# Performance work log

Measured on AMD Instinct MI355X. Metric: run time of the kernel, lower is better.

## Reference

```python
import jax, jax.numpy as jnp
import numpy as np

B = 4096
D = 512
TEMPERATURE = 0.07


def setup_inputs() -> dict:
    key = jax.random.key(0)
    k1, k2 = jax.random.split(key)
    logits = jax.random.normal(k1, (B, D), dtype=jnp.float32)
    label = jax.random.normal(k2, (B, D), dtype=jnp.float32)
    return {"logits": logits, "label": label}


def reference(logits, label):
    # concat the two views -> [2B, D]
    feats = jnp.concatenate([logits, label], axis=0)
    n = feats.shape[0]
    b = n // 2
    # L2 normalize along feature dim (F.normalize, eps for safety)
    norm = jnp.maximum(jnp.linalg.norm(feats, axis=1, keepdims=True), 1e-12)
    feats = feats / norm
    # similarity matrix [2B, 2B]
    sim = jnp.matmul(feats, feats.T) / TEMPERATURE
    idx = jnp.arange(n)
    # positive pair of row i is row (i + B) mod 2B
    pos = sim[idx, (idx + b) % n]
    # CrossEntropy with target 0 over [pos, negatives] == masked LSE - pos.
    # Mask out the diagonal (self-similarity), which the torch code removes
    # via the boolean-eye mask before building logits.
    neg_inf = jnp.array(-jnp.inf, dtype=sim.dtype)
    sim_masked = jnp.where(idx[:, None] == idx[None, :], neg_inf, sim)
    lse = jax.nn.logsumexp(sim_masked, axis=1)
    loss = jnp.mean(lse - pos)
    return loss
```

## Files before the change

### kernel.cpp

```cpp
#include <hip/hip_runtime.h>
#include <hip/hip_bf16.h>

#define NROWS 8192
#define BHALF 4096
#define DDIM  512

#define BM 256
#define BK 64
#define KT (DDIM / BK)
#define NT (NROWS / BM)
#define NTRI (NT * (NT + 1) / 2)
#define NFULL 512
#define NHALFB 32
#define GRID (NFULL + NHALFB)

#define FSCALE 3.7796447300922722f

typedef short bf16x8 __attribute__((ext_vector_type(8)));
typedef float f32x4 __attribute__((ext_vector_type(4)));
typedef unsigned short u16x8 __attribute__((ext_vector_type(8)));
typedef __attribute__((address_space(1))) unsigned int gu32;
typedef __attribute__((address_space(3))) unsigned int lu32;

#define MFMA_(a, b, c) __builtin_amdgcn_mfma_f32_16x16x32_bf16(a, b, c, 0, 0, 0)
#define VMCNT(N) asm volatile("s_waitcnt vmcnt(" #N ")" ::: "memory")
#define LGKM0                                            \
  do {                                                   \
    asm volatile("s_waitcnt lgkmcnt(0)" ::: "memory");   \
    __builtin_amdgcn_sched_barrier(0);                   \
  } while (0)
#define BAR                                              \
  do {                                                   \
    __builtin_amdgcn_sched_barrier(0);                   \
    __builtin_amdgcn_s_barrier();                        \
    __builtin_amdgcn_sched_barrier(0);                   \
  } while (0)

__global__ __launch_bounds__(256) void normalize_kernel(
    const float* __restrict__ logits, const float* __restrict__ label,
    unsigned short* __restrict__ fn, float* __restrict__ rowsum,
    float* __restrict__ out) {
  if (blockIdx.x < 8)
    ((float4*)rowsum)[blockIdx.x * 256 + threadIdx.x] =
        make_float4(0.f, 0.f, 0.f, 0.f);
  if (blockIdx.x == 8 && threadIdx.x == 0) out[0] = 0.f;

  const int w = threadIdx.x >> 6, lane = threadIdx.x & 63;
  const int row = blockIdx.x * 4 + w;
  const float* src = (row < BHALF) ? (logits + (size_t)row * DDIM)
                                   : (label + (size_t)(row - BHALF) * DDIM);
  const float4* s4 = (const float4*)src;
  float4 a = s4[lane * 2 + 0];
  float4 b = s4[lane * 2 + 1];
  float ss = a.x * a.x + a.y * a.y + a.z * a.z + a.w * a.w +
             b.x * b.x + b.y * b.y + b.z * b.z + b.w * b.w;
#pragma unroll
  for (int m = 1; m < 64; m <<= 1) ss += __shfl_xor(ss, m);
  const float inv = FSCALE / fmaxf(sqrtf(ss), 1e-12f);
  const float v[8] = {a.x, a.y, a.z, a.w, b.x, b.y, b.z, b.w};
  u16x8 o;
#pragma unroll
  for (int j = 0; j < 8; ++j) {
    float x = v[j] * inv;
    unsigned u = __float_as_uint(x);
    unsigned r = (u + 0x7fffu + ((u >> 16) & 1u)) >> 16;
    o[j] = (unsigned short)r;
  }
  *(u16x8*)(fn + (size_t)row * DDIM + lane * 8) = o;
}

template <int BN_>
__device__ __attribute__((always_inline)) void tile_body(
    const unsigned short* __restrict__ fn, float* __restrict__ rowsum,
    float* __restrict__ pos, int rowBase, int colBase) {
  extern __shared__ char lds[];
  __shared__ float lds_rsum[BM];
  __shared__ float lds_csum[BM];
  constexpr int NFRAG = BN_ / 64;
  constexpr int BUFSZ = 32768 + BN_ * 128;

  const int tid = threadIdx.x;
  const int w = tid >> 6, lane = tid & 63;
  const int wr = w >> 2, wc = w & 3;
  const int l15 = lane & 15, l4 = lane >> 4;
  const int r8 = lane >> 3;
  const int sw16 = ((lane & 7) ^ r8) << 4;

  if (tid < BM) {
    lds_rsum[tid] = 0.f;
    lds_csum[tid] = 0.f;
  }

  auto stageA = [&](int d, int kk, int R) {
    const char* g =
        (const char*)(fn + (size_t)(rowBase + R + w * 8 + r8) * DDIM + kk) + sw16;
    __builtin_amdgcn_global_load_lds(
        (gu32*)g, (lu32*)(lds + d * BUFSZ + (R + w * 8) * 128), 16, 0, 0);
  };
  auto stageB = [&](int d, int kk, int R) {
    const char* g =
        (const char*)(fn + (size_t)(colBase + R + w * 8 + r8) * DDIM + kk) + sw16;
    __builtin_amdgcn_global_load_lds(
        (gu32*)g, (lu32*)(lds + d * BUFSZ + 32768 + (R + w * 8) * 128), 16, 0, 0);
  };
  auto readA = [&](int d, int m, int ks) -> bf16x8 {
    const int r = wr * 128 + m * 16 + l15;
    return *(const bf16x8*)(lds + d * BUFSZ + r * 128 +
                            (((ks * 4 + l4) ^ (r & 7)) << 4));
  };
  auto readB = [&](int d, int n, int ks) -> bf16x8 {
    const int r = wc * (BN_ / 4) + n * 16 + l15;
    return *(const bf16x8*)(lds + d * BUFSZ + 32768 + r * 128 +
                            (((ks * 4 + l4) ^ (r & 7)) << 4));
  };

  f32x4 acc[8][NFRAG];
#pragma unroll
  for (int m = 0; m < 8; ++m)
#pragma unroll
    for (int n = 0; n < NFRAG; ++n) acc[m][n] = (f32x4){0.f, 0.f, 0.f, 0.f};

#define PHASE0(STAGES)                                                    \
  {                                                                       \
    _Pragma("unroll") for (int n = 0; n < NFRAG; ++n) {                   \
      bf[n][0] = readB(d, n, 0);                                          \
      bf[n][1] = readB(d, n, 1);                                          \
    }                                                                     \
    bf16x8 a00 = readA(d, 0, 0), a01 = readA(d, 0, 1);                    \
    bf16x8 a10 = readA(d, 1, 0), a11 = readA(d, 1, 1);                    \
    STAGES;                                                               \
    BAR;                                                                  \
    LGKM0;                                                                \
    __builtin_amdgcn_s_setprio(1);                                        \
    _Pragma("unroll") for (int n = 0; n < NFRAG; ++n) {                   \
      acc[0][n] = MFMA_(a00, bf[n][0], acc[0][n]);                        \
      acc[1][n] = MFMA_(a10, bf[n][0], acc[1][n]);                        \
    }                                                                     \
    _Pragma("unroll") for (int n = 0; n < NFRAG; ++n) {                   \
      acc[0][n] = MFMA_(a01, bf[n][1], acc[0][n]);                        \
      acc[1][n] = MFMA_(a11, bf[n][1], acc[1][n]);                        \
    }                                                                     \
    __builtin_amdgcn_s_setprio(0);                                        \
    BAR;                                                                  \
  }

#define PHASE(P, STAGES, TAILWAIT)                                        \
  {                                                                       \
    bf16x8 a00 = readA(d, 2 * (P), 0), a01 = readA(d, 2 * (P), 1);        \
    bf16x8 a10 = readA(d, 2 * (P) + 1, 0), a11 = readA(d, 2 * (P) + 1, 1);\
    STAGES;                                                               \
    BAR;                                                                  \
    LGKM0;                                                                \
    __builtin_amdgcn_s_setprio(1);                                        \
    _Pragma("unroll") for (int n = 0; n < NFRAG; ++n) {                   \
      acc[2 * (P)][n] = MFMA_(a00, bf[n][0], acc[2 * (P)][n]);            \
      acc[2 * (P) + 1][n] = MFMA_(a10, bf[n][0], acc[2 * (P) + 1][n]);    \
    }                                                                     \
    _Pragma("unroll") for (int n = 0; n < NFRAG; ++n) {                   \
      acc[2 * (P)][n] = MFMA_(a01, bf[n][1], acc[2 * (P)][n]);            \
      acc[2 * (P) + 1][n] = MFMA_(a11, bf[n][1], acc[2 * (P) + 1][n]);    \
    }                                                                     \
    __builtin_amdgcn_s_setprio(0);                                        \
    TAILWAIT;                                                             \
    BAR;                                                                  \
  }

  stageB(0, 0, 0);
  stageB(0, 0, 64);
  if constexpr (BN_ == 256) {
    stageB(0, 0, 128);
    stageB(0, 0, 192);
  }
  stageA(0, 0, 0);
  stageA(0, 0, 128);
  stageA(0, 0, 64);
  stageA(0, 0, 192);
  VMCNT(2);
  BAR;

  for (int t = 0; t < KT - 1; ++t) {
    const int d = t & 1, o = d ^ 1;
    const int kn = (t + 1) * BK;
    bf16x8 bf[NFRAG][2];
    PHASE0(stageB(o, kn, 0); stageB(o, kn, 64));
    if constexpr (BN_ == 256) {
      PHASE(1, stageB(o, kn, 128); stageB(o, kn, 192), VMCNT(4));
    } else {
      PHASE(1, (void)0, VMCNT(2));
    }
    PHASE(2, stageA(o, kn, 0); stageA(o, kn, 128), (void)0);
    PHASE(3, stageA(o, kn, 64); stageA(o, kn, 192), VMCNT(2));
  }
  {
    const int d = (KT - 1) & 1;
    bf16x8 bf[NFRAG][2];
    PHASE0((void)0);
    PHASE(1, (void)0, VMCNT(0));
    PHASE(2, (void)0, (void)0);
    PHASE(3, (void)0, (void)0);
  }
#undef PHASE0
#undef PHASE

  float rs[8][4];
  float cs[NFRAG];
#pragma unroll
  for (int m = 0; m < 8; ++m)
#pragma unroll
    for (int j = 0; j < 4; ++j) rs[m][j] = 0.f;
#pragma unroll
  for (int n = 0; n < NFRAG; ++n) cs[n] = 0.f;

#pragma unroll
  for (int m = 0; m < 8; ++m)
#pragma unroll
    for (int n = 0; n < NFRAG; ++n)
#pragma unroll
      for (int j = 0; j < 4; ++j) {
        const int rl = wr * 128 + m * 16 + l4 * 4 + j;
        const int cl = wc * (BN_ / 4) + n * 16 + l15;
        const int grow = rowBase + rl, gcol = colBase + cl;
        const float v = acc[m][n][j];
        float e = __expf(v);
        if (grow == gcol) e = 0.f;
        rs[m][j] += e;
        cs[n] += e;
        if (gcol == grow + BHALF) pos[grow] = v;
      }

#pragma unroll
  for (int m = 0; m < 8; ++m)
#pragma unroll
    for (int j = 0; j < 4; ++j) {
      float s = rs[m][j];
      s += __shfl_xor(s, 1);
      s += __shfl_xor(s, 2);
      s += __shfl_xor(s, 4);
      s += __shfl_xor(s, 8);
      if (l15 == 0) atomicAdd(&lds_rsum[wr * 128 + m * 16 + l4 * 4 + j], s);
    }
  if (rowBase != colBase) {
#pragma unroll
    for (int n = 0; n < NFRAG; ++n) {
      float s = cs[n];
      s += __shfl_xor(s, 16);
      s += __shfl_xor(s, 32);
      if (l4 == 0) atomicAdd(&lds_csum[wc * (BN_ / 4) + n * 16 + l15], s);
    }
  }
  __syncthreads();
  if (tid < BM) atomicAdd(&rowsum[rowBase + tid], lds_rsum[tid]);
  if (rowBase != colBase && tid < BN_)
    atomicAdd(&rowsum[colBase + tid], lds_csum[tid]);
}

__global__ __launch_bounds__(512) void simexp_tri_kernel(
    const unsigned short* __restrict__ fn, float* __restrict__ rowsum,
    float* __restrict__ pos) {
  const int bid = (int)blockIdx.x;
  const bool half = (bid >= NFULL);
  int beta, colOff = 0;
  if (!half) {
    const int b = (bid & 7) * (NFULL / 8) + (bid >> 3);
    beta = (b == 1) ? 527 : b;
  } else {
    const int hb = bid - NFULL;
    const int t = NFULL + (hb >> 1);
    beta = (t == 527) ? 1 : t;
    colOff = (hb & 1) * 128;
  }
  int k = (int)((sqrtf(8.f * (float)beta + 1.f) - 1.f) * 0.5f);
  while ((k + 1) * (k + 2) / 2 <= beta) ++k;
  while (k * (k + 1) / 2 > beta) --k;
  const int rm = (NT - 1) - k;
  const int cn = (NT - 1) - (beta - k * (k + 1) / 2);
  const int rowBase = rm * BM, colBase = cn * BM + colOff;

  if (!half)
    tile_body<256>(fn, rowsum, pos, rowBase, colBase);
  else
    tile_body<128>(fn, rowsum, pos, rowBase, colBase);
}

__global__ __launch_bounds__(256) void reduce_kernel(
    const float* __restrict__ rowsum, const float* __restrict__ pos,
    float* __restrict__ out) {
  __shared__ float part[4];
  const int i = blockIdx.x * 256 + threadIdx.x;
  float a = __logf(rowsum[i]) - pos[i & (BHALF - 1)];
#pragma unroll
  for (int m = 1; m < 64; m <<= 1) a += __shfl_xor(a, m);
  const int w = threadIdx.x >> 6, lane = threadIdx.x & 63;
  if (lane == 0) part[w] = a;
  __syncthreads();
  if (threadIdx.x == 0)
    atomicAdd(out, (part[0] + part[1] + part[2] + part[3]) * (1.0f / NROWS));
}

extern "C" void kernel_launch(void* const* d_in, const int* in_sizes, int n_in,
                              void* d_out, int out_size, void* d_ws, size_t ws_size,
                              hipStream_t stream) {
  const float* logits = (const float*)d_in[0];
  const float* label = (const float*)d_in[1];
  float* out = (float*)d_out;
  unsigned short* fn = (unsigned short*)d_ws;
  float* rowsum = (float*)((char*)d_ws + (size_t)NROWS * DDIM * 2);
  float* pos = rowsum + NROWS;

  normalize_kernel<<<NROWS / 4, 256, 0, stream>>>(logits, label, fn, rowsum, out);
  simexp_tri_kernel<<<GRID, 512, 2 * 65536, stream>>>(fn, rowsum, pos);
  reduce_kernel<<<NROWS / 256, 256, 0, stream>>>(rowsum, pos, out);
}
```

Measured before the change: 124.5 us.

## Split tail tiles into quarter-width blocks and issue all stage loads in phase zero

The leftover triangle tiles (the last 16 diagonal-ish tiles) are now split into four 64-column blocks instead of two 128-column blocks, so 64 extra workgroups share the tail work. This is meant to shorten the last wave and reduce load imbalance. The double-buffer prefetch also changes: all B and A stage loads for the next k-step are issued at once in phase 0, with the vmcnt waits adjusted, instead of being spread across the four phases. Issuing everything up front may raise memory-queue pressure and register use, and it changes how the loads overlap with the MFMA work. The smaller tiles also reuse loaded data less.

```diff
diff --git a/kernel.cpp b/kernel.cpp
--- a/kernel.cpp
+++ b/kernel.cpp
@@ -11,8 +11,8 @@
 #define NT (NROWS / BM)
 #define NTRI (NT * (NT + 1) / 2)
 #define NFULL 512
-#define NHALFB 32
-#define GRID (NFULL + NHALFB)
+#define NQB 64
+#define GRID (NFULL + NQB)
 
 #define FSCALE 3.7796447300922722f
 
@@ -144,11 +144,10 @@
     BAR;                                                                  \
   }
 
-#define PHASE(P, STAGES, TAILWAIT)                                        \
+#define PHASE(P, TAILWAIT)                                                \
   {                                                                       \
     bf16x8 a00 = readA(d, 2 * (P), 0), a01 = readA(d, 2 * (P), 1);        \
     bf16x8 a10 = readA(d, 2 * (P) + 1, 0), a11 = readA(d, 2 * (P) + 1, 1);\
-    STAGES;                                                               \
     BAR;                                                                  \
     LGKM0;                                                                \
     __builtin_amdgcn_s_setprio(1);                                        \
@@ -165,11 +164,10 @@
     BAR;                                                                  \
   }
 
-  stageB(0, 0, 0);
-  stageB(0, 0, 64);
   if constexpr (BN_ == 256) {
-    stageB(0, 0, 128);
-    stageB(0, 0, 192);
+    stageB(0, 0, 0); stageB(0, 0, 64); stageB(0, 0, 128); stageB(0, 0, 192);
+  } else {
+    stageB(0, 0, 0);
   }
   stageA(0, 0, 0);
   stageA(0, 0, 128);
@@ -182,22 +180,26 @@
     const int d = t & 1, o = d ^ 1;
     const int kn = (t + 1) * BK;
     bf16x8 bf[NFRAG][2];
-    PHASE0(stageB(o, kn, 0); stageB(o, kn, 64));
     if constexpr (BN_ == 256) {
-      PHASE(1, stageB(o, kn, 128); stageB(o, kn, 192), VMCNT(4));
+      PHASE0(stageB(o, kn, 0); stageB(o, kn, 64); stageB(o, kn, 128);
+             stageB(o, kn, 192); stageA(o, kn, 0); stageA(o, kn, 128);
+             stageA(o, kn, 64); stageA(o, kn, 192));
+      PHASE(1, VMCNT(8));
     } else {
-      PHASE(1, (void)0, VMCNT(2));
+      PHASE0(stageB(o, kn, 0); stageA(o, kn, 0); stageA(o, kn, 128);
+             stageA(o, kn, 64); stageA(o, kn, 192));
+      PHASE(1, VMCNT(5));
     }
-    PHASE(2, stageA(o, kn, 0); stageA(o, kn, 128), (void)0);
-    PHASE(3, stageA(o, kn, 64); stageA(o, kn, 192), VMCNT(2));
+    PHASE(2, (void)0);
+    PHASE(3, VMCNT(2));
   }
   {
     const int d = (KT - 1) & 1;
     bf16x8 bf[NFRAG][2];
     PHASE0((void)0);
-    PHASE(1, (void)0, VMCNT(0));
-    PHASE(2, (void)0, (void)0);
-    PHASE(3, (void)0, (void)0);
+    PHASE(1, VMCNT(0));
+    PHASE(2, (void)0);
+    PHASE(3, (void)0);
   }
 #undef PHASE0
 #undef PHASE
@@ -258,16 +260,16 @@
     const unsigned short* __restrict__ fn, float* __restrict__ rowsum,
     float* __restrict__ pos) {
   const int bid = (int)blockIdx.x;
-  const bool half = (bid >= NFULL);
+  const bool quarter = (bid >= NFULL);
   int beta, colOff = 0;
-  if (!half) {
+  if (!quarter) {
     const int b = (bid & 7) * (NFULL / 8) + (bid >> 3);
     beta = (b == 1) ? 527 : b;
   } else {
-    const int hb = bid - NFULL;
-    const int t = NFULL + (hb >> 1);
+    const int qb = bid - NFULL;
+    const int t = NFULL + (qb >> 2);
     beta = (t == 527) ? 1 : t;
-    colOff = (hb & 1) * 128;
+    colOff = (qb & 3) * 64;
   }
   int k = (int)((sqrtf(8.f * (float)beta + 1.f) - 1.f) * 0.5f);
   while ((k + 1) * (k + 2) / 2 <= beta) ++k;
@@ -276,10 +278,10 @@
   const int cn = (NT - 1) - (beta - k * (k + 1) / 2);
   const int rowBase = rm * BM, colBase = cn * BM + colOff;
 
-  if (!half)
+  if (!quarter)
     tile_body<256>(fn, rowsum, pos, rowBase, colBase);
   else
-    tile_body<128>(fn, rowsum, pos, rowBase, colBase);
+    tile_body<64>(fn, rowsum, pos, rowBase, colBase);
 }
 
 __global__ __launch_bounds__(256) void reduce_kernel(
```

New measurement: 124.7 us. No clear change (+0.2%).
